# Kernel tuning notes

Measured on AMD Instinct MI355X. Metric: run time of the kernel, lower is better.

The kernel has to match this reference:

```python
import jax, jax.numpy as jnp
import numpy as np

B, C_IN, H, W = 4, 512, 188, 188
SHARED_CH = 64
NUM_CLASS = 3
M = 200
NUM_MAX = 500
STRIDE = 8
PCR = (-75.2, -75.2, -2.0, 75.2, 75.2, 4.0)
VOX = (0.1, 0.1, 0.15)
OUT_CH = (2, 1, 3, 2, 1, 3)  # center, center_z, dim, rot, iou, hm
MIN_RADIUS = 2.0
OVERLAP = 0.1
INIT_BIAS = -2.19


def conv3x3(x, w):
    return jax.lax.conv_general_dilated(x, w, (1, 1), 'SAME',
                                        dimension_numbers=('NCHW', 'OIHW', 'NCHW'))


def bn_relu(x, p):
    # p: [4, C] = gamma, beta, running_mean, running_var (inference-mode BN)
    g, b, m, v = p[0], p[1], p[2], p[3]
    scale = (g * jax.lax.rsqrt(v + 1e-5))[None, :, None, None]
    y = (x - m[None, :, None, None]) * scale + b[None, :, None, None]
    return jax.nn.relu(y)


def gaussian_radius(height, width, min_overlap):
    # Faithful to OpenPCDet centernet_utils.gaussian_radius
    b1 = height + width
    c1 = width * height * (1 - min_overlap) / (1 + min_overlap)
    sq1 = jnp.sqrt(jnp.maximum(b1 * b1 - 4.0 * c1, 0.0))
    r1 = (b1 + sq1) / 2.0
    b2 = 2.0 * (height + width)
    c2 = (1 - min_overlap) * width * height
    sq2 = jnp.sqrt(jnp.maximum(b2 * b2 - 16.0 * c2, 0.0))
    r2 = (b2 + sq2) / 2.0
    a3 = 4.0 * min_overlap
    b3 = -2.0 * min_overlap * (height + width)
    c3 = (min_overlap - 1.0) * width * height
    sq3 = jnp.sqrt(jnp.maximum(b3 * b3 - 4.0 * a3 * c3, 0.0))
    r3 = (b3 + sq3) / 2.0
    return jnp.minimum(jnp.minimum(r1, r2), r3)


def assign_targets(gt_boxes):
    # gt_boxes: [B, M, 8] = x, y, z, dx, dy, dz, heading, class(1..NUM_CLASS)
    x, y, z = gt_boxes[..., 0], gt_boxes[..., 1], gt_boxes[..., 2]
    dx, dy, dz = gt_boxes[..., 3], gt_boxes[..., 4], gt_boxes[..., 5]
    heading = gt_boxes[..., 6]
    cls = jax.lax.stop_gradient(gt_boxes[..., 7]).astype(jnp.int32)

    cx = jnp.clip((x - PCR[0]) / VOX[0] / STRIDE, 0.0, W - 0.5)  # [B,M]
    cy = jnp.clip((y - PCR[1]) / VOX[1] / STRIDE, 0.0, H - 0.5)
    cxi = jax.lax.stop_gradient(jnp.floor(cx)).astype(jnp.int32)  # .int() trunc == floor (>=0)
    cyi = jax.lax.stop_gradient(jnp.floor(cy)).astype(jnp.int32)

    dxp = dx / VOX[0] / STRIDE
    dyp = dy / VOX[1] / STRIDE
    r = gaussian_radius(dxp, dyp, OVERLAP)
    r = jnp.maximum(jnp.floor(jax.lax.stop_gradient(r)), MIN_RADIUS)  # clamp_min(r.int(), 2)
    sigma = (2.0 * r + 1.0) / 6.0
    valid = (dx > 0) & (dy > 0)  # [B,M]

    ox = jnp.arange(W, dtype=jnp.int32)[None, None, :] - cxi[..., None]  # [B,M,W]
    oy = jnp.arange(H, dtype=jnp.int32)[None, None, :] - cyi[..., None]  # [B,M,H]
    d2 = (oy.astype(jnp.float32) ** 2)[:, :, :, None] + (ox.astype(jnp.float32) ** 2)[:, :, None, :]
    g = jnp.exp(-d2 / (2.0 * sigma * sigma)[:, :, None, None])  # [B,M,H,W]
    win = (jnp.abs(oy)[:, :, :, None] <= r[:, :, None, None]) & \
          (jnp.abs(ox)[:, :, None, :] <= r[:, :, None, None])
    g = jnp.where(win & valid[:, :, None, None], g, 0.0)

    # per-class max-splat (draw_gaussian_to_heatmap uses torch.max overlap)
    heatmap = jnp.stack(
        [jnp.max(jnp.where((cls == c + 1)[:, :, None, None], g, 0.0), axis=1)
         for c in range(NUM_CLASS)], axis=1)  # [B,NUM_CLASS,H,W]

    vf = valid.astype(gt_boxes.dtype)
    vals = jnp.stack([cx - cxi.astype(cx.dtype), cy - cyi.astype(cy.dtype), z,
                      jnp.log(dx), jnp.log(dy), jnp.log(dz),
                      jnp.cos(heading), jnp.sin(heading)], axis=-1) * vf[..., None]
    target_boxes = jnp.zeros((B, NUM_MAX, 8), gt_boxes.dtype).at[:, :M].set(vals)
    ind_vals = (cyi * W + cxi) * valid.astype(jnp.int32)
    inds = jnp.zeros((B, NUM_MAX), jnp.int32).at[:, :M].set(ind_vals)
    mask = jnp.zeros((B, NUM_MAX), jnp.int32).at[:, :M].set(valid.astype(jnp.int32))
    return heatmap, target_boxes, inds, mask


def setup_inputs() -> dict:
    key = jax.random.key(0)
    ks = jax.random.split(key, 16)
    spatial_features = jax.random.normal(ks[0], (B, C_IN, H, W), jnp.float32)
    x = jax.random.uniform(ks[1], (B, M), minval=-70.0, maxval=70.0)
    y = jax.random.uniform(ks[2], (B, M), minval=-70.0, maxval=70.0)
    z = jax.random.uniform(ks[3], (B, M), minval=-1.0, maxval=1.0)
    dx = jax.random.uniform(ks[4], (B, M), minval=1.5, maxval=5.0)
    dy = jax.random.uniform(ks[5], (B, M), minval=1.5, maxval=5.0)
    dz = jax.random.uniform(ks[6], (B, M), minval=1.0, maxval=3.0)
    hd = jax.random.uniform(ks[7], (B, M), minval=-np.pi, maxval=np.pi)
    cls = jax.random.randint(ks[8], (B, M), 1, NUM_CLASS + 1).astype(jnp.float32)
    gt_boxes = jnp.stack([x, y, z, dx, dy, dz, hd, cls], axis=-1)

    def mk_bn(k, lead):
        kk = jax.random.split(k, 4)
        g = 1.0 + 0.1 * jax.random.normal(kk[0], lead + (SHARED_CH,))
        b = 0.1 * jax.random.normal(kk[1], lead + (SHARED_CH,))
        m = 0.1 * jax.random.normal(kk[2], lead + (SHARED_CH,))
        v = jax.random.uniform(kk[3], lead + (SHARED_CH,), minval=0.5, maxval=1.5)
        return jnp.stack([g, b, m, v], axis=len(lead))

    w_shared = jax.random.normal(ks[9], (SHARED_CH, C_IN, 3, 3)) * (1.0 / np.sqrt(C_IN * 9))
    bn_shared = mk_bn(ks[10], ())
    w1_heads = jax.random.normal(ks[11], (6, SHARED_CH, SHARED_CH, 3, 3)) * (1.0 / np.sqrt(SHARED_CH * 9))
    bn_heads = mk_bn(ks[12], (6,))
    w2_heads = jax.random.normal(ks[13], (6, 3, SHARED_CH, 3, 3)) * (1.0 / np.sqrt(SHARED_CH * 9))
    b2_heads = jnp.zeros((6, 3), jnp.float32).at[5].set(INIT_BIAS)  # hm branch bias = -2.19
    return {'spatial_features': spatial_features, 'gt_boxes': gt_boxes,
            'w_shared': w_shared, 'bn_shared': bn_shared,
            'w1_heads': w1_heads, 'bn_heads': bn_heads,
            'w2_heads': w2_heads, 'b2_heads': b2_heads}


def reference(spatial_features, gt_boxes, w_shared, bn_shared,
              w1_heads, bn_heads, w2_heads, b2_heads):
    shared = bn_relu(conv3x3(spatial_features, w_shared), bn_shared)  # [B,64,H,W]

    def branch(w1, bnp, w2, b2):
        h = bn_relu(conv3x3(shared, w1), bnp)
        return conv3x3(h, w2) + b2[None, :, None, None]  # [B,3,H,W] (out padded to 3)

    outs = jax.vmap(branch)(w1_heads, bn_heads, w2_heads, b2_heads)  # [6,B,3,H,W]
    head_out = jnp.concatenate([outs[i, :, :OUT_CH[i]] for i in range(6)], axis=1)  # [B,12,H,W]

    heatmap, target_boxes, inds, mask = assign_targets(gt_boxes)
    return head_out, heatmap, target_boxes, inds, mask
```

## Files before the change

kernel.cpp:

```cpp
#include <hip/hip_runtime.h>
#include <hip/hip_bf16.h>

#define HWD 188
#define NPX (HWD*HWD)
#define NB 4
#define CIN 512
#define CH 64
#define MBOX 200
#define NMAX 500

#define HEAD_SZ (NB*12*NPX)
#define HM_OFF  HEAD_SZ
#define TB_OFF  (HM_OFF + NB*3*NPX)
#define IND_OFF (TB_OFF + NB*NMAX*8)
#define MSK_OFF (IND_OFF + NB*NMAX)

typedef short sh8 __attribute__((ext_vector_type(8)));
typedef float f4 __attribute__((ext_vector_type(4)));
typedef unsigned short us4 __attribute__((ext_vector_type(4)));

__device__ __constant__ int d_cum[6]  = {0, 2, 3, 6, 8, 9};
__device__ __constant__ int d_outc[6] = {2, 1, 3, 2, 1, 3};

__device__ __forceinline__ unsigned short bf16_bits(float v) {
  union { __hip_bfloat16 h; unsigned short u; } cv;
  cv.h = __float2bfloat16(v);
  return cv.u;
}

__device__ __forceinline__ int xcd_swz(int bid, int grid) {
  return (bid & 7) * (grid >> 3) + (bid >> 3);
}

__global__ __launch_bounds__(256) void wprep(
    const float* __restrict__ ws_, const float* __restrict__ w1_,
    const float* __restrict__ w2_, unsigned short* __restrict__ w1b,
    unsigned short* __restrict__ w2b, unsigned short* __restrict__ w3b) {
  int e = blockIdx.x * 256 + threadIdx.x;
  const int N1 = 9 * 16 * 64 * 32;
  const int N2 = 6 * 9 * 64 * 64;
  const int N3 = 6 * 9 * 16 * 64;
  if (e < N1) {
    int icr = e & 31; int r1 = e >> 5;
    int oc = r1 & 63; int r2 = r1 >> 6;
    int icq = r2 & 15; int tap = r2 >> 4;
    w1b[e] = bf16_bits(ws_[(oc * 512 + icq * 32 + icr) * 9 + tap]);
  } else if (e < N1 + N2) {
    int f = e - N1;
    int h = f / (9 * 64 * 64); int r = f % (9 * 64 * 64);
    int tap = r / (64 * 64); int r2 = r % (64 * 64);
    int oc = r2 / 64; int ic = r2 % 64;
    w2b[f] = bf16_bits(w1_[((h * 64 + oc) * 64 + ic) * 9 + tap]);
  } else if (e < N1 + N2 + N3) {
    int f = e - N1 - N2;
    int h = f / (9 * 16 * 64); int r = f % (9 * 16 * 64);
    int tap = r / (16 * 64); int r2 = r % (16 * 64);
    int oc = r2 / 64; int ic = r2 % 64;
    float v = (oc < 3) ? w2_[((h * 3 + oc) * 64 + ic) * 9 + tap] : 0.f;
    w3b[f] = bf16_bits(v);
  }
}

#define C1_PXS 40
#define C1_LDS (10*18*C1_PXS)
__global__ __launch_bounds__(256, 4) void conv1_mfma(
    const float* __restrict__ sf,
    const unsigned short* __restrict__ wb,
    const float* __restrict__ bnp,
    unsigned short* __restrict__ outp) {
  __shared__ __align__(16) short s_in[2][C1_LDS];
  const int t = threadIdx.x;
  const int swz = xcd_swz(blockIdx.x, 1152);
  const int b = swz / 288;
  const int tt = swz % 288;
  const int y0 = (tt / 12) * 8, x0 = (tt % 12) * 16;
  const int w = t >> 6, lane = t & 63, ln = lane & 15, kg = lane >> 4;
  const int rg = w & 1, og = w >> 1;

  const bool st_act = (t < 240);
  const int icg = t & 3, cg = (t >> 2) % 6, sr = (t >> 2) / 6;
  const int gy_s = y0 - 1 + sr;
  const int gx0_s = x0 - 4 + cg * 4;
  const bool row_ok = (gy_s >= 0 && gy_s < HWD);
  const bool vec_ok = (gx0_s >= 0 && gx0_s + 3 < HWD);
  const float* sbase = sf + (((long long)b * CIN + icg * 8) * HWD + gy_s) * HWD + gx0_s;

  f4 acc[2][4];
#pragma unroll
  for (int i = 0; i < 2; ++i)
#pragma unroll
    for (int j = 0; j < 4; ++j) acc[i][j] = (f4){0.f, 0.f, 0.f, 0.f};

  f4 st[8];
#pragma unroll
  for (int j = 0; j < 8; ++j) st[j] = (f4){0.f, 0.f, 0.f, 0.f};

#define C1_LOAD(IC0)                                                        \
  do {                                                                      \
    if (st_act && row_ok) {                                                 \
      const float* p = sbase + (long long)(IC0) * NPX;                      \
      if (vec_ok) {                                                         \
        _Pragma("unroll")                                                   \
        for (int j = 0; j < 8; ++j)                                         \
          st[j] = *reinterpret_cast<const f4*>(p + (long long)j * NPX);     \
      } else {                                                              \
        _Pragma("unroll")                                                   \
        for (int j = 0; j < 8; ++j) st[j] = (f4){0.f, 0.f, 0.f, 0.f};       \
        _Pragma("unroll")                                                   \
        for (int k = 0; k < 4; ++k) {                                       \
          int gx = gx0_s + k;                                               \
          if (gx >= 0 && gx < HWD) {                                        \
            _Pragma("unroll")                                               \
            for (int j = 0; j < 8; ++j) st[j][k] = p[(long long)j * NPX + k];\
          }                                                                 \
        }                                                                   \
      }                                                                     \
    } else {                                                                \
      _Pragma("unroll")                                                     \
      for (int j = 0; j < 8; ++j) st[j] = (f4){0.f, 0.f, 0.f, 0.f};         \
    }                                                                       \
  } while (0)

#define C1_WRITE(BUF)                                                       \
  do {                                                                      \
    if (st_act) {                                                           \
      _Pragma("unroll")                                                     \
      for (int k = 0; k < 4; ++k) {                                         \
        int col = cg * 4 + k - 3;                                           \
        if ((unsigned)col < 18u) {                                          \
          sh8 pk;                                                           \
          _Pragma("unroll")                                                 \
          for (int j = 0; j < 8; ++j) pk[j] = (short)bf16_bits(st[j][k]);   \
          *reinterpret_cast<sh8*>(&(BUF)[(sr * 18 + col) * C1_PXS + icg * 8]) = pk; \
        }                                                                   \
      }                                                                     \
    }                                                                       \
  } while (0)

  C1_LOAD(0);
  C1_WRITE(s_in[0]);
  __syncthreads();

  for (int s = 0; s < 16; ++s) {
    const short* cur = s_in[s & 1];
    if (s < 15) C1_LOAD((s + 1) * 32);
    __builtin_amdgcn_s_setprio(1);
#pragma unroll
    for (int tap = 0; tap < 9; ++tap) {
      const int ky = tap / 3, kx = tap % 3;
      sh8 af[2];
#pragma unroll
      for (int i = 0; i < 2; ++i)
        af[i] = *reinterpret_cast<const sh8*>(
            wb + (((tap * 16 + s) * 64) + (2 * og + i) * 16 + ln) * 32 + kg * 8);
#pragma unroll
      for (int nt = 0; nt < 4; ++nt) {
        const int rr = 4 * rg + nt + ky;
        const int cc = ln + kx;
        sh8 bf = *reinterpret_cast<const sh8*>(&cur[(rr * 18 + cc) * C1_PXS + kg * 8]);
#pragma unroll
        for (int i = 0; i < 2; ++i)
          acc[i][nt] = __builtin_amdgcn_mfma_f32_16x16x32_bf16(
              af[i], bf, acc[i][nt], 0, 0, 0);
      }
    }
    __builtin_amdgcn_s_setprio(0);
    if (s < 15) C1_WRITE(s_in[(s & 1) ^ 1]);
    __syncthreads();
  }

#pragma unroll
  for (int i = 0; i < 2; ++i) {
    const int ocb = (2 * og + i) * 16 + kg * 4;
    f4 g4 = *reinterpret_cast<const f4*>(bnp + ocb);
    f4 b4 = *reinterpret_cast<const f4*>(bnp + 64 + ocb);
    f4 m4 = *reinterpret_cast<const f4*>(bnp + 128 + ocb);
    f4 v4 = *reinterpret_cast<const f4*>(bnp + 192 + ocb);
    f4 sc, bi;
#pragma unroll
    for (int j = 0; j < 4; ++j) {
      sc[j] = g4[j] * rsqrtf(v4[j] + 1e-5f);
      bi[j] = b4[j] - m4[j] * sc[j];
    }
#pragma unroll
    for (int nt = 0; nt < 4; ++nt) {
      int y = y0 + 4 * rg + nt;
      int x = x0 + ln;
      if (y < HWD && x < HWD) {
        us4 pk;
#pragma unroll
        for (int j = 0; j < 4; ++j)
          pk[j] = bf16_bits(fmaxf(acc[i][nt][j] * sc[j] + bi[j], 0.f));
        *reinterpret_cast<us4*>(outp + (((long long)b * HWD + y) * HWD + x) * 64 + ocb) = pk;
      }
    }
  }
#undef C1_LOAD
#undef C1_WRITE
}

#define SB_PXS 40
__global__ __launch_bounds__(256, 3) void conv23_fused(
    const unsigned short* __restrict__ inp,
    const unsigned short* __restrict__ w2b,
    const unsigned short* __restrict__ w3b,
    const float* __restrict__ bnH,
    const float* __restrict__ b2,
    float* __restrict__ hout) {
  __shared__ __align__(16) short s_in[240 * 72];
  __shared__ __align__(16) short s_buf[180 * SB_PXS];
  const int t = threadIdx.x;
  const int swz = xcd_swz(blockIdx.x, 6912);
  const int h = swz % 6;
  const int tile = swz / 6;
  const int b = tile / 288;
  const int tt = tile % 288;
  const int y0 = (tt / 12) * 8, x0 = (tt % 12) * 16;
  const int w = t >> 6, lane = t & 63, ln = lane & 15, kg = lane >> 4;

  for (int idx = t; idx < 1920; idx += 256) {
    int ch8 = idx & 7; int px = idx >> 3;
    int r = (px * 205) >> 12; int c = px - r * 20;
    int gy = y0 - 2 + r, gx = x0 - 2 + c;
    sh8 v = (sh8){0, 0, 0, 0, 0, 0, 0, 0};
    if (gy >= 0 && gy < HWD && gx >= 0 && gx < HWD)
      v = *reinterpret_cast<const sh8*>(
          &inp[(((long long)b * HWD + gy) * HWD + gx) * 64 + ch8 * 8]);
    *reinterpret_cast<sh8*>(&s_in[px * 72 + ch8 * 8]) = v;
  }

  int ibase[3], qaddr[3];
  bool wr_ok[3], img_ok[3];
#pragma unroll
  for (int nt = 0; nt < 3; ++nt) {
    int q = (w * 3 + nt) * 16 + ln;
    wr_ok[nt] = (q < 180);
    if (q > 179) q = 179;
    int r2 = (q * 57) >> 10; int c2 = q - r2 * 18;
    ibase[nt] = (r2 * 20 + c2) * 72 + kg * 8;
    qaddr[nt] = q;
    int gy2 = y0 - 1 + r2, gx2 = x0 - 1 + c2;
    img_ok[nt] = (gy2 >= 0 && gy2 < HWD && gx2 >= 0 && gx2 < HWD);
  }
  int b3base[2], oy[2], ox[2];
#pragma unroll
  for (int nt = 0; nt < 2; ++nt) {
    int p = (w * 2 + nt) * 16 + ln;
    int r3 = p >> 4, c3 = p & 15;
    b3base[nt] = ((r3 + 1) * 18 + (c3 + 1)) * SB_PXS + kg * 8;
    oy[nt] = y0 + r3; ox[nt] = x0 + c3;
  }

  const float* bnp = bnH + h * 256;
  f4 acc3[2];
#pragma unroll
  for (int j = 0; j < 2; ++j) acc3[j] = (f4){0.f, 0.f, 0.f, 0.f};

  __syncthreads();

#pragma unroll
  for (int O = 0; O < 2; ++O) {
    f4 acc2[2][3];
#pragma unroll
    for (int i = 0; i < 2; ++i)
#pragma unroll
      for (int j = 0; j < 3; ++j) acc2[i][j] = (f4){0.f, 0.f, 0.f, 0.f};
#pragma unroll
    for (int icq = 0; icq < 2; ++icq) {
      sh8 af[2][9];
#pragma unroll
      for (int tap = 0; tap < 9; ++tap)
#pragma unroll
        for (int mt = 0; mt < 2; ++mt)
          af[mt][tap] = *reinterpret_cast<const sh8*>(
              w2b + (((h * 9 + tap) * 64) + O * 32 + mt * 16 + ln) * 64 + icq * 32 + kg * 8);
      __builtin_amdgcn_s_setprio(1);
#pragma unroll
      for (int tap = 0; tap < 9; ++tap) {
        const int ky = tap / 3, kx = tap % 3;
        const int toff = (ky * 20 + kx) * 72 + icq * 32;
#pragma unroll
        for (int nt = 0; nt < 3; ++nt) {
          sh8 bf = *reinterpret_cast<const sh8*>(&s_in[ibase[nt] + toff]);
#pragma unroll
          for (int mt = 0; mt < 2; ++mt)
            acc2[mt][nt] = __builtin_amdgcn_mfma_f32_16x16x32_bf16(
                af[mt][tap], bf, acc2[mt][nt], 0, 0, 0);
        }
      }
      __builtin_amdgcn_s_setprio(0);
    }
#pragma unroll
    for (int mt = 0; mt < 2; ++mt) {
      const int ocb = O * 32 + mt * 16 + kg * 4;
      f4 g4 = *reinterpret_cast<const f4*>(bnp + ocb);
      f4 b4 = *reinterpret_cast<const f4*>(bnp + 64 + ocb);
      f4 m4 = *reinterpret_cast<const f4*>(bnp + 128 + ocb);
      f4 v4 = *reinterpret_cast<const f4*>(bnp + 192 + ocb);
      f4 sc, bi;
#pragma unroll
      for (int j = 0; j < 4; ++j) {
        sc[j] = g4[j] * rsqrtf(v4[j] + 1e-5f);
        bi[j] = b4[j] - m4[j] * sc[j];
      }
#pragma unroll
      for (int nt = 0; nt < 3; ++nt) {
        if (wr_ok[nt]) {
          us4 pk = {0, 0, 0, 0};
          if (img_ok[nt]) {
#pragma unroll
            for (int j = 0; j < 4; ++j)
              pk[j] = bf16_bits(fmaxf(acc2[mt][nt][j] * sc[j] + bi[j], 0.f));
          }
          *reinterpret_cast<us4*>(&s_buf[qaddr[nt] * SB_PXS + mt * 16 + kg * 4]) = pk;
        }
      }
    }
    __syncthreads();
    sh8 af3[9];
#pragma unroll
    for (int tap = 0; tap < 9; ++tap)
      af3[tap] = *reinterpret_cast<const sh8*>(
          w3b + (((h * 9 + tap) * 16) + ln) * 64 + O * 32 + kg * 8);
    __builtin_amdgcn_s_setprio(1);
#pragma unroll
    for (int tap = 0; tap < 9; ++tap) {
      const int dy = tap / 3 - 1, dx = tap % 3 - 1;
      const int toff = (dy * 18 + dx) * SB_PXS;
#pragma unroll
      for (int nt = 0; nt < 2; ++nt) {
        sh8 bf3 = *reinterpret_cast<const sh8*>(&s_buf[b3base[nt] + toff]);
        acc3[nt] = __builtin_amdgcn_mfma_f32_16x16x32_bf16(af3[tap], bf3, acc3[nt], 0, 0, 0);
      }
    }
    __builtin_amdgcn_s_setprio(0);
    if (O == 0) __syncthreads();
  }

  const int c_off = d_cum[h], noc = d_outc[h];
#pragma unroll
  for (int nt = 0; nt < 2; ++nt) {
    if (oy[nt] < HWD && ox[nt] < HWD) {
#pragma unroll
      for (int j = 0; j < 4; ++j) {
        int oc = kg * 4 + j;
        if (oc < noc)
          hout[((long long)b * 12 + c_off + oc) * NPX + oy[nt] * HWD + ox[nt]] =
              acc3[nt][j] + b2[h * 3 + oc];
      }
    }
  }
}

__global__ __launch_bounds__(256) void targets_kernel(
    const float* __restrict__ gt, float* __restrict__ out, float* __restrict__ boxp) {
  int idx = blockIdx.x * 256 + threadIdx.x;
  if (idx >= NB * NMAX) return;
  int b = idx / NMAX, j = idx - b * NMAX;
  float vals[8] = {0, 0, 0, 0, 0, 0, 0, 0};
  float indf = 0.f, mkf = 0.f;
  if (j < MBOX) {
    const float* g = gt + (b * MBOX + j) * 8;
    float x = g[0], y = g[1], z = g[2], dx = g[3], dy = g[4], dz = g[5];
    float hd = g[6], cls = g[7];
    float cx = (x - (-75.2f)) / 0.1f / 8.0f;
    cx = fminf(fmaxf(cx, 0.0f), (float)HWD - 0.5f);
    float cy = (y - (-75.2f)) / 0.1f / 8.0f;
    cy = fminf(fmaxf(cy, 0.0f), (float)HWD - 0.5f);
    float cxf = floorf(cx), cyf = floorf(cy);
    int cxi = (int)cxf, cyi = (int)cyf;
    float hh = dx / 0.1f / 8.0f;
    float ww = dy / 0.1f / 8.0f;
    const float ov = 0.1f;
    float b1 = hh + ww;
    float c1 = ww * hh * (1.0f - ov) / (1.0f + ov);
    float sq1 = sqrtf(fmaxf(b1 * b1 - 4.0f * c1, 0.0f));
    float r1 = (b1 + sq1) / 2.0f;
    float b2_ = 2.0f * (hh + ww);
    float c2 = (1.0f - ov) * ww * hh;
    float sq2 = sqrtf(fmaxf(b2_ * b2_ - 16.0f * c2, 0.0f));
    float r2 = (b2_ + sq2) / 2.0f;
    float a3 = 4.0f * ov;
    float b3 = -2.0f * ov * (hh + ww);
    float c3 = (ov - 1.0f) * ww * hh;
    float sq3 = sqrtf(fmaxf(b3 * b3 - 4.0f * a3 * c3, 0.0f));
    float r3 = (b3 + sq3) / 2.0f;
    float r = fminf(fminf(r1, r2), r3);
    r = fmaxf(floorf(r), 2.0f);
    float sigma = (2.0f * r + 1.0f) / 6.0f;
    float inv2s2 = 1.0f / (2.0f * sigma * sigma);
    bool valid = (dx > 0.0f) && (dy > 0.0f);
    float vf = valid ? 1.0f : 0.0f;
    vals[0] = (cx - cxf) * vf;
    vals[1] = (cy - cyf) * vf;
    vals[2] = z * vf;
    vals[3] = logf(dx) * vf;
    vals[4] = logf(dy) * vf;
    vals[5] = logf(dz) * vf;
    vals[6] = cosf(hd) * vf;
    vals[7] = sinf(hd) * vf;
    indf = (float)((cyi * HWD + cxi) * (valid ? 1 : 0));
    mkf = vf;
    float* bp = boxp + (b * MBOX + j) * 8;
    bp[0] = cxf; bp[1] = cyf; bp[2] = r; bp[3] = inv2s2;
    bp[4] = valid ? cls : 0.0f; bp[5] = 0.f; bp[6] = 0.f; bp[7] = 0.f;
  }
  float* tb = out + TB_OFF + (b * NMAX + j) * 8;
#pragma unroll
  for (int k = 0; k < 8; ++k) tb[k] = vals[k];
  out[IND_OFF + b * NMAX + j] = indf;
  out[MSK_OFF + b * NMAX + j] = mkf;
}

__global__ __launch_bounds__(256) void heatmap_kernel(
    const float* __restrict__ boxp, float* __restrict__ out) {
  __shared__ float s_bp[MBOX][5];
  const int t = threadIdx.x, b = blockIdx.y;
  for (int e = t; e < MBOX * 5; e += 256) {
    int j = e / 5, k = e - j * 5;
    s_bp[j][k] = boxp[(b * MBOX + j) * 8 + k];
  }
  __syncthreads();
  int p = blockIdx.x * 256 + t;
  if (p >= NPX) return;
  int y = p / HWD, x = p - y * HWD;
  float a0 = 0.f, a1 = 0.f, a2 = 0.f;
  for (int j = 0; j < MBOX; ++j) {
    int c = (int)s_bp[j][4];
    if (c == 0) continue;
    float ox = (float)x - s_bp[j][0];
    float oy = (float)y - s_bp[j][1];
    float r = s_bp[j][2];
    if (fabsf(ox) <= r && fabsf(oy) <= r) {
      float gg = expf(-(ox * ox + oy * oy) * s_bp[j][3]);
      if (c == 1) a0 = fmaxf(a0, gg);
      else if (c == 2) a1 = fmaxf(a1, gg);
      else a2 = fmaxf(a2, gg);
    }
  }
  int base = HM_OFF + (b * 3 * HWD + y) * HWD + x;
  out[base] = a0;
  out[base + NPX] = a1;
  out[base + 2 * NPX] = a2;
}

extern "C" void kernel_launch(void* const* d_in, const int* in_sizes, int n_in,
                              void* d_out, int out_size, void* d_ws, size_t ws_size,
                              hipStream_t stream) {
  (void)in_sizes; (void)n_in; (void)out_size; (void)ws_size;
  const float* sf = (const float*)d_in[0];
  const float* gt = (const float*)d_in[1];
  const float* w_shared = (const float*)d_in[2];
  const float* bn_shared = (const float*)d_in[3];
  const float* w1 = (const float*)d_in[4];
  const float* bnH = (const float*)d_in[5];
  const float* w2 = (const float*)d_in[6];
  const float* b2 = (const float*)d_in[7];
  float* out = (float*)d_out;
  char* ws = (char*)d_ws;

  const size_t SH = (size_t)NB * NPX * 64 * 2;
  unsigned short* shared_t = (unsigned short*)ws;
  unsigned short* w1b = (unsigned short*)(ws + SH);
  unsigned short* w2b = (unsigned short*)(ws + SH + 589824);
  unsigned short* w3b = (unsigned short*)(ws + SH + 589824 + 442368);
  float* boxp = (float*)(ws + SH + 589824 + 442368 + 110592);

  wprep<<<2232, 256, 0, stream>>>(w_shared, w1, w2, w1b, w2b, w3b);

  conv1_mfma<<<1152, 256, 0, stream>>>(sf, w1b, bn_shared, shared_t);

  conv23_fused<<<6912, 256, 0, stream>>>(shared_t, w2b, w3b, bnH, b2, out);

  targets_kernel<<<(NB * NMAX + 255) / 256, 256, 0, stream>>>(gt, out, boxp);
  heatmap_kernel<<<dim3((NPX + 255) / 256, NB), 256, 0, stream>>>(boxp, out);
}
```

Baseline: 596.8 us.

## Loop all six heads inside one block per tile to reuse the staged input

```diff
diff --git a/kernel.cpp b/kernel.cpp
--- a/kernel.cpp
+++ b/kernel.cpp
@@ -199,67 +199,58 @@
 #undef C1_WRITE
 }
 
-#define SB_PXS 40
-__global__ __launch_bounds__(256, 3) void conv23_fused(
+__global__ __launch_bounds__(512, 4) void conv23_fused(
     const unsigned short* __restrict__ inp,
     const unsigned short* __restrict__ w2b,
     const unsigned short* __restrict__ w3b,
     const float* __restrict__ bnH,
     const float* __restrict__ b2,
     float* __restrict__ hout) {
-  __shared__ __align__(16) short s_in[240 * 72];
-  __shared__ __align__(16) short s_buf[180 * SB_PXS];
+  __shared__ __align__(16) short s_in[8 * 240 * 8];
+  __shared__ __align__(16) short s_buf[8 * 180 * 8];
   const int t = threadIdx.x;
-  const int swz = xcd_swz(blockIdx.x, 6912);
-  const int h = swz % 6;
-  const int tile = swz / 6;
-  const int b = tile / 288;
-  const int tt = tile % 288;
+  const int swz = xcd_swz(blockIdx.x, 1152);
+  const int b = swz / 288;
+  const int tt = swz % 288;
   const int y0 = (tt / 12) * 8, x0 = (tt % 12) * 16;
   const int w = t >> 6, lane = t & 63, ln = lane & 15, kg = lane >> 4;
-
-  for (int idx = t; idx < 1920; idx += 256) {
-    int ch8 = idx & 7; int px = idx >> 3;
-    int r = (px * 205) >> 12; int c = px - r * 20;
-    int gy = y0 - 2 + r, gx = x0 - 2 + c;
-    sh8 v = (sh8){0, 0, 0, 0, 0, 0, 0, 0};
-    if (gy >= 0 && gy < HWD && gx >= 0 && gx < HWD)
-      v = *reinterpret_cast<const sh8*>(
-          &inp[(((long long)b * HWD + gy) * HWD + gx) * 64 + ch8 * 8]);
-    *reinterpret_cast<sh8*>(&s_in[px * 72 + ch8 * 8]) = v;
-  }
-
-  int ibase[3], qaddr[3];
+  const int og = w & 1, pg = w >> 1;
+
+#pragma unroll
+  for (int k = 0; k < 4; ++k) {
+    int idx = t + k * 512;
+    if (idx < 1920) {
+      int g = idx / 240, px = idx - (idx / 240) * 240;
+      int r = px / 20, c = px - (px / 20) * 20;
+      int gy = y0 - 2 + r, gx = x0 - 2 + c;
+      sh8 v = (sh8){0, 0, 0, 0, 0, 0, 0, 0};
+      if (gy >= 0 && gy < HWD && gx >= 0 && gx < HWD)
+        v = *reinterpret_cast<const sh8*>(
+            &inp[(((long long)b * HWD + gy) * HWD + gx) * 64 + g * 8]);
+      *reinterpret_cast<sh8*>(&s_in[(g * 240 + px) * 8]) = v;
+    }
+  }
+
+  int ibase_px[3], qpx[3];
   bool wr_ok[3], img_ok[3];
 #pragma unroll
   for (int nt = 0; nt < 3; ++nt) {
-    int q = (w * 3 + nt) * 16 + ln;
+    int q = (pg * 3 + nt) * 16 + ln;
     wr_ok[nt] = (q < 180);
     if (q > 179) q = 179;
-    int r2 = (q * 57) >> 10; int c2 = q - r2 * 18;
-    ibase[nt] = (r2 * 20 + c2) * 72 + kg * 8;
-    qaddr[nt] = q;
+    int r2 = q / 18, c2 = q - (q / 18) * 18;
+    ibase_px[nt] = r2 * 20 + c2;
+    qpx[nt] = q;
     int gy2 = y0 - 1 + r2, gx2 = x0 - 1 + c2;
     img_ok[nt] = (gy2 >= 0 && gy2 < HWD && gx2 >= 0 && gx2 < HWD);
   }
-  int b3base[2], oy[2], ox[2];
-#pragma unroll
-  for (int nt = 0; nt < 2; ++nt) {
-    int p = (w * 2 + nt) * 16 + ln;
-    int r3 = p >> 4, c3 = p & 15;
-    b3base[nt] = ((r3 + 1) * 18 + (c3 + 1)) * SB_PXS + kg * 8;
-    oy[nt] = y0 + r3; ox[nt] = x0 + c3;
-  }
-
-  const float* bnp = bnH + h * 256;
-  f4 acc3[2];
-#pragma unroll
-  for (int j = 0; j < 2; ++j) acc3[j] = (f4){0.f, 0.f, 0.f, 0.f};
+  const int b3px = (w + 1) * 18 + (ln + 1);
+  const int oyy = y0 + w, oxx = x0 + ln;
+  const bool out_ok = (oyy < HWD && oxx < HWD);
 
   __syncthreads();
 
-#pragma unroll
-  for (int O = 0; O < 2; ++O) {
+  for (int h = 0; h < 6; ++h) {
     f4 acc2[2][3];
 #pragma unroll
     for (int i = 0; i < 2; ++i)
@@ -267,42 +258,42 @@
       for (int j = 0; j < 3; ++j) acc2[i][j] = (f4){0.f, 0.f, 0.f, 0.f};
 #pragma unroll
     for (int icq = 0; icq < 2; ++icq) {
-      sh8 af[2][9];
-#pragma unroll
-      for (int tap = 0; tap < 9; ++tap)
-#pragma unroll
-        for (int mt = 0; mt < 2; ++mt)
-          af[mt][tap] = *reinterpret_cast<const sh8*>(
-              w2b + (((h * 9 + tap) * 64) + O * 32 + mt * 16 + ln) * 64 + icq * 32 + kg * 8);
       __builtin_amdgcn_s_setprio(1);
 #pragma unroll
       for (int tap = 0; tap < 9; ++tap) {
         const int ky = tap / 3, kx = tap % 3;
-        const int toff = (ky * 20 + kx) * 72 + icq * 32;
+        const int toff = ky * 20 + kx;
+        sh8 af0 = *reinterpret_cast<const sh8*>(
+            w2b + (((h * 9 + tap) * 64) + og * 32 + ln) * 64 + icq * 32 + kg * 8);
+        sh8 af1 = *reinterpret_cast<const sh8*>(
+            w2b + (((h * 9 + tap) * 64) + og * 32 + 16 + ln) * 64 + icq * 32 + kg * 8);
 #pragma unroll
         for (int nt = 0; nt < 3; ++nt) {
-          sh8 bf = *reinterpret_cast<const sh8*>(&s_in[ibase[nt] + toff]);
-#pragma unroll
-          for (int mt = 0; mt < 2; ++mt)
-            acc2[mt][nt] = __builtin_amdgcn_mfma_f32_16x16x32_bf16(
-                af[mt][tap], bf, acc2[mt][nt], 0, 0, 0);
+          sh8 bf = *reinterpret_cast<const sh8*>(
+              &s_in[((icq * 4 + kg) * 240 + ibase_px[nt] + toff) * 8]);
+          acc2[0][nt] = __builtin_amdgcn_mfma_f32_16x16x32_bf16(af0, bf, acc2[0][nt], 0, 0, 0);
+          acc2[1][nt] = __builtin_amdgcn_mfma_f32_16x16x32_bf16(af1, bf, acc2[1][nt], 0, 0, 0);
         }
       }
       __builtin_amdgcn_s_setprio(0);
     }
+    __syncthreads();
+    const float* bnp = bnH + h * 256;
 #pragma unroll
     for (int mt = 0; mt < 2; ++mt) {
-      const int ocb = O * 32 + mt * 16 + kg * 4;
-      f4 g4 = *reinterpret_cast<const f4*>(bnp + ocb);
-      f4 b4 = *reinterpret_cast<const f4*>(bnp + 64 + ocb);
-      f4 m4 = *reinterpret_cast<const f4*>(bnp + 128 + ocb);
-      f4 v4 = *reinterpret_cast<const f4*>(bnp + 192 + ocb);
+      const int cch = og * 32 + mt * 16 + kg * 4;
+      f4 g4 = *reinterpret_cast<const f4*>(bnp + cch);
+      f4 b4 = *reinterpret_cast<const f4*>(bnp + 64 + cch);
+      f4 m4 = *reinterpret_cast<const f4*>(bnp + 128 + cch);
+      f4 v4 = *reinterpret_cast<const f4*>(bnp + 192 + cch);
       f4 sc, bi;
 #pragma unroll
       for (int j = 0; j < 4; ++j) {
         sc[j] = g4[j] * rsqrtf(v4[j] + 1e-5f);
         bi[j] = b4[j] - m4[j] * sc[j];
       }
+      const int g8 = cch >> 3;
+      const int off = cch & 7;
 #pragma unroll
       for (int nt = 0; nt < 3; ++nt) {
         if (wr_ok[nt]) {
@@ -312,41 +303,34 @@
             for (int j = 0; j < 4; ++j)
               pk[j] = bf16_bits(fmaxf(acc2[mt][nt][j] * sc[j] + bi[j], 0.f));
           }
-          *reinterpret_cast<us4*>(&s_buf[qaddr[nt] * SB_PXS + mt * 16 + kg * 4]) = pk;
+          *reinterpret_cast<us4*>(&s_buf[(g8 * 180 + qpx[nt]) * 8 + off]) = pk;
         }
       }
     }
     __syncthreads();
-    sh8 af3[9];
-#pragma unroll
-    for (int tap = 0; tap < 9; ++tap)
-      af3[tap] = *reinterpret_cast<const sh8*>(
-          w3b + (((h * 9 + tap) * 16) + ln) * 64 + O * 32 + kg * 8);
+    f4 acc3 = (f4){0.f, 0.f, 0.f, 0.f};
     __builtin_amdgcn_s_setprio(1);
 #pragma unroll
-    for (int tap = 0; tap < 9; ++tap) {
-      const int dy = tap / 3 - 1, dx = tap % 3 - 1;
-      const int toff = (dy * 18 + dx) * SB_PXS;
-#pragma unroll
-      for (int nt = 0; nt < 2; ++nt) {
-        sh8 bf3 = *reinterpret_cast<const sh8*>(&s_buf[b3base[nt] + toff]);
-        acc3[nt] = __builtin_amdgcn_mfma_f32_16x16x32_bf16(af3[tap], bf3, acc3[nt], 0, 0, 0);
+    for (int kq = 0; kq < 2; ++kq) {
+#pragma unroll
+      for (int tap = 0; tap < 9; ++tap) {
+        const int dy = tap / 3 - 1, dx = tap % 3 - 1;
+        sh8 af3 = *reinterpret_cast<const sh8*>(
+            w3b + (((h * 9 + tap) * 16) + ln) * 64 + kq * 32 + kg * 8);
+        sh8 bf3 = *reinterpret_cast<const sh8*>(
+            &s_buf[((kq * 4 + kg) * 180 + b3px + dy * 18 + dx) * 8]);
+        acc3 = __builtin_amdgcn_mfma_f32_16x16x32_bf16(af3, bf3, acc3, 0, 0, 0);
       }
     }
     __builtin_amdgcn_s_setprio(0);
-    if (O == 0) __syncthreads();
-  }
-
-  const int c_off = d_cum[h], noc = d_outc[h];
-#pragma unroll
-  for (int nt = 0; nt < 2; ++nt) {
-    if (oy[nt] < HWD && ox[nt] < HWD) {
+    const int c_off = d_cum[h], noc = d_outc[h];
+    if (out_ok) {
 #pragma unroll
       for (int j = 0; j < 4; ++j) {
         int oc = kg * 4 + j;
         if (oc < noc)
-          hout[((long long)b * 12 + c_off + oc) * NPX + oy[nt] * HWD + ox[nt]] =
-              acc3[nt][j] + b2[h * 3 + oc];
+          hout[((long long)b * 12 + c_off + oc) * NPX + oyy * HWD + oxx] =
+              acc3[j] + b2[h * 3 + oc];
       }
     }
   }
@@ -470,7 +454,7 @@
 
   conv1_mfma<<<1152, 256, 0, stream>>>(sf, w1b, bn_shared, shared_t);
 
-  conv23_fused<<<6912, 256, 0, stream>>>(shared_t, w2b, w3b, bnH, b2, out);
+  conv23_fused<<<1152, 512, 0, stream>>>(shared_t, w2b, w3b, bnH, b2, out);
 
   targets_kernel<<<(NB * NMAX + 255) / 256, 256, 0, stream>>>(gt, out, boxp);
   heatmap_kernel<<<dim3((NPX + 255) / 256, NB), 256, 0, stream>>>(boxp, out);
```

New measurement: 703.9 us. 17.9% more time.
